# Kernel optimization log

Hardware: AMD Instinct MI355X
Metric: run time of the kernel (lower is better)

Reference implementation:

```python
import jax, jax.numpy as jnp
import numpy as np

E = 6          # num_experts
TOP_K = 2
FUT = 60       # future_len
DIM = 128

def _gelu(x):
    return jax.nn.gelu(x, approximate=False)  # torch nn.GELU default is exact erf


def setup_inputs() -> dict:
    key = jax.random.key(0)
    ks = jax.random.split(key, 20)
    B, M, D = 8192, 6, DIM
    s = 0.02
    inp = {
        "mode_features": jax.random.normal(ks[0], (B, M, D), jnp.float32),
        # router MLP: D->256->128->E  (dropout is identity in eval mode)
        "rW1": jax.random.normal(ks[1], (D, 256)) * s, "rb1": jnp.zeros((256,)),
        "rW2": jax.random.normal(ks[2], (256, 128)) * s, "rb2": jnp.zeros((128,)),
        "rW3": jax.random.normal(ks[3], (128, E)) * s, "rb3": jnp.zeros((E,)),
        # stacked expert trajectory heads: D->256->256->2*FUT
        "tW1": jax.random.normal(ks[4], (E, D, 256)) * s, "tb1": jnp.zeros((E, 256)),
        "tW2": jax.random.normal(ks[5], (E, 256, 256)) * s, "tb2": jnp.zeros((E, 256)),
        "tW3": jax.random.normal(ks[6], (E, 256, 2 * FUT)) * s, "tb3": jnp.zeros((E, 2 * FUT)),
        # stacked expert score heads: D->128->64->1
        "sW1": jax.random.normal(ks[7], (E, D, 128)) * s, "sb1": jnp.zeros((E, 128)),
        "sW2": jax.random.normal(ks[8], (E, 128, 64)) * s, "sb2": jnp.zeros((E, 64)),
        "sW3": jax.random.normal(ks[9], (E, 64, 1)) * s, "sb3": jnp.zeros((E, 1)),
    }
    return {k: v.astype(jnp.float32) for k, v in inp.items()}


def reference(mode_features, rW1, rb1, rW2, rb2, rW3, rb3,
              tW1, tb1, tW2, tb2, tW3, tb3,
              sW1, sb1, sW2, sb2, sW3, sb3):
    B, M, D = mode_features.shape
    x = mode_features.reshape(B * M, D)  # [N, D]

    # ---- router (dropout = identity at inference) ----
    h = _gelu(x @ rW1 + rb1)
    h = _gelu(h @ rW2 + rb2)
    logits = h @ rW3 + rb3                      # [N, E]
    router_probs = jax.nn.softmax(logits, axis=-1)

    top_v, top_i = jax.lax.top_k(logits, TOP_K)  # [N, K]
    top_w = jax.nn.softmax(top_v, axis=-1)       # renormalized top-k weights

    # ---- all experts, dense over E (then gather top-k) ----
    th = _gelu(jnp.einsum('nd,edh->neh', x, tW1) + tb1)   # [N, E, 256]
    th = _gelu(jnp.einsum('neh,ehg->neg', th, tW2) + tb2) # [N, E, 256]
    traj_all = jnp.einsum('neh,eho->neo', th, tW3) + tb3  # [N, E, 2*FUT]

    sh = _gelu(jnp.einsum('nd,edh->neh', x, sW1) + sb1)   # [N, E, 128]
    sh = _gelu(jnp.einsum('neh,ehg->neg', sh, sW2) + sb2) # [N, E, 64]
    score_all = (jnp.einsum('neh,eho->neo', sh, sW3) + sb3)[..., 0]  # [N, E]

    traj_sel = jnp.take_along_axis(traj_all, top_i[:, :, None], axis=1)  # [N, K, 2*FUT]
    score_sel = jnp.take_along_axis(score_all, top_i, axis=1)            # [N, K]

    trajectories = (top_w[:, :, None] * traj_sel).sum(axis=1).reshape(B, M, FUT, 2)
    scores = (top_w * score_sel).sum(axis=1).reshape(B, M)

    # ---- load-balance aux loss ----
    avg_probs = router_probs.mean(axis=0)  # [E]
    entropy = -(avg_probs * jnp.log(avg_probs + 1e-8)).sum()
    lb_loss = -entropy * 0.01
    l2_loss = jnp.mean((avg_probs - 1.0 / E) ** 2)
    aux_loss = lb_loss + 0.01 * l2_loss

    return trajectories, scores, aux_loss, router_probs.reshape(B, M, E)
```

## Files before the change

kernel.cpp:

```cpp
#include <hip/hip_runtime.h>

#define N_TOK 49152
#define PER_E 155648
#define NSTAGE 19
#define RSTAGES 24

#define TRAJ_OFF 0
#define SCORE_OFF 5898240
#define AUX_OFF  5947392
#define PROB_OFF 5947393

typedef __attribute__((ext_vector_type(8))) short short8v;
typedef __attribute__((ext_vector_type(4))) float f32x4;
typedef __attribute__((ext_vector_type(4))) unsigned short u16x4;

typedef __attribute__((address_space(3))) unsigned char lds_byte;
typedef __attribute__((address_space(1))) const unsigned char gl_byte;

__device__ __forceinline__ unsigned short f2bf(float f) {
  unsigned int u = __float_as_uint(f);
  u = (u + 0x7FFFu + ((u >> 16) & 1u)) >> 16;
  return (unsigned short)u;
}
__device__ __forceinline__ float bf2f(unsigned short h) {
  return __uint_as_float(((unsigned int)h) << 16);
}
__device__ __forceinline__ float geluf(float v) {
  float x = v * 0.70710678118654752f;
  float ax = fabsf(x);
  float t = __builtin_amdgcn_rcpf(fmaf(0.3275911f, ax, 1.0f));
  float p = t * fmaf(t, fmaf(t, fmaf(t, fmaf(t, 1.061405429f, -1.453152027f),
                                     1.421413741f), -0.284496736f), 0.254829592f);
  float er = 1.0f - p * __expf(-ax * ax);
  er = copysignf(er, x);
  return 0.5f * v * (1.0f + er);
}

__global__ __launch_bounds__(256) void prep_weights(
    const float* __restrict__ tW1, const float* __restrict__ tW2, const float* __restrict__ tW3,
    const float* __restrict__ sW1, const float* __restrict__ sW2,
    unsigned short* __restrict__ blob)
{
  int id = blockIdx.x * 256 + threadIdx.x;
  if (id >= 6 * PER_E) return;
  int e = id / PER_E;
  int r = id - e * PER_E;
  int p = r >> 13;
  int q = r & 8191;
  int f = q >> 9;
  int l = (q >> 3) & 63;
  int j = q & 7;
  int hi = l >> 4, rl = l & 15;
  const float* src; int N, tile, ks; bool perm;
  if (p < 2)       { src = sW1 + e * 16384; N = 128; tile = 4 * p + (f >> 2);        ks = f & 3; perm = false; }
  else if (p == 2) { src = sW2 + e * 8192;  N = 64;  tile = f >> 2;                  ks = f & 3; perm = true;  }
  else if (p < 7)  { src = tW1 + e * 32768; N = 256; tile = 4 * (p - 3) + (f >> 2);  ks = f & 3; perm = false; }
  else if (p < 11) { src = tW2 + e * 65536; N = 256; tile = 2 * (p - 7) + (f >> 3);  ks = f & 7; perm = true;  }
  else if (p < 13) { src = tW3 + e * 30720; N = 120; tile = f >> 1;  ks = 2 * (p - 11) + (f & 1); perm = true; }
  else if (p < 17) { src = tW2 + e * 65536; N = 256; tile = 8 + 2 * (p - 13) + (f >> 3); ks = f & 7; perm = true; }
  else             { src = tW3 + e * 30720; N = 120; tile = f >> 1;  ks = 4 + 2 * (p - 17) + (f & 1); perm = true; }
  int k = ks * 32 + (perm ? (16 * (j >> 2) + 4 * hi + (j & 3)) : (8 * hi + j));
  int unit = tile * 16 + rl;
  blob[id] = f2bf(unit < N ? src[k * N + unit] : 0.0f);
}

__global__ __launch_bounds__(256) void prep_router(
    const float* __restrict__ rW1, const float* __restrict__ rW2,
    unsigned short* __restrict__ rblob)
{
  int id = blockIdx.x * 256 + threadIdx.x;
  if (id >= RSTAGES * 8192) return;
  int p = id >> 13;
  int q = id & 8191;
  int f = q >> 9;
  int l = (q >> 3) & 63;
  int j = q & 7;
  int hi = l >> 4, rl = l & 15;
  const float* src; int N, tile, ks, part; bool perm;
  if (p < 12) { int c = p / 3; part = p % 3; src = rW1; N = 256; tile = 4 * c + (f >> 2); ks = f & 3; perm = false; }
  else        { int c = (p - 12) / 3; part = (p - 12) % 3; src = rW2; N = 128; tile = 2 * c + (f >> 3); ks = f & 7; perm = true; }
  int k = ks * 32 + (perm ? (16 * (j >> 2) + 4 * hi + (j & 3)) : (8 * hi + j));
  int unit = tile * 16 + rl;
  float v = (unit < N) ? src[k * N + unit] : 0.0f;
  unsigned short b0 = f2bf(v);
  float r1 = v - bf2f(b0);
  unsigned short b1 = f2bf(r1);
  float r2 = r1 - bf2f(b1);
  unsigned short b2 = f2bf(r2);
  rblob[id] = (part == 0) ? b0 : ((part == 1) ? b1 : b2);
}

__device__ __forceinline__ f32x4 MM16(short8v a, short8v b, f32x4 c) {
  return __builtin_amdgcn_mfma_f32_16x16x32_bf16(a, b, c, 0, 0, 0);
}
__device__ __forceinline__ void cvt16(f32x4 aE, f32x4 aO, const float* bp, int hi, short8v& fr) {
  #pragma unroll
  for (int j = 0; j < 8; ++j) {
    float v = (j < 4) ? aE[j & 3] : aO[j & 3];
    int unit = 16 * (j >> 2) + 4 * hi + (j & 3);
    fr[j] = (short)f2bf(geluf(v + bp[unit]));
  }
}
__device__ __forceinline__ void cvt16s(f32x4 aE, f32x4 aO, const float* bp, int hi,
                                       short8v& f0, short8v& f1) {
  #pragma unroll
  for (int j = 0; j < 8; ++j) {
    float v = (j < 4) ? aE[j & 3] : aO[j & 3];
    int unit = 16 * (j >> 2) + 4 * hi + (j & 3);
    float g = geluf(v + bp[unit]);
    unsigned short b0 = f2bf(g);
    f0[j] = (short)b0;
    f1[j] = (short)f2bf(g - bf2f(b0));
  }
}

#define FRAG(s, f) (*(const short8v*)(&wlds[((s) % 3) * 8192 + (f) * 512 + lane * 8]))

#define RSTAGE(s) do { \
    const unsigned short* gsrc_ = rblob + (s) * 8192 + w * 1024 + lane * 8; \
    unsigned short* ldst_ = &wlds[((s) % 3) * 8192 + w * 1024]; \
    _Pragma("unroll") \
    for (int i_ = 0; i_ < 2; ++i_) \
      __builtin_amdgcn_global_load_lds((gl_byte*)(gsrc_ + i_ * 512), (lds_byte*)(ldst_ + i_ * 512), 16, 0, 0); \
  } while (0)

#define RPIPE(s, nw) do { \
    asm volatile("s_waitcnt vmcnt(" #nw ")" ::: "memory"); \
    __builtin_amdgcn_sched_barrier(0); \
    __builtin_amdgcn_s_barrier(); \
    __builtin_amdgcn_sched_barrier(0); \
    if ((s) + 2 < RSTAGES) RSTAGE((s) + 2); \
  } while (0)

__global__ __launch_bounds__(512, 4) void router_mfma(
    const float* __restrict__ x, const unsigned short* __restrict__ rblob,
    const float* __restrict__ rb1, const float* __restrict__ rb2,
    const float* __restrict__ rW3, const float* __restrict__ rb3,
    float* __restrict__ probs_out,
    int* __restrict__ pairTok, float* __restrict__ pairW, int* __restrict__ pairIdx,
    int* __restrict__ cnt, float* __restrict__ probsum)
{
  __shared__ __align__(16) unsigned short wlds[3 * 8192];
  __shared__ float bLds[1160];
  __shared__ float probsLds[768];
  __shared__ float psum[8];
  __shared__ int lcnt[8], gbase[8];

  int tid = threadIdx.x;
  int lane = tid & 63;
  int w = tid >> 6;
  int col = lane & 15;
  int hi = lane >> 4;
  int tok0 = blockIdx.x * 128;
  int myTok = tok0 + w * 16 + col;

  if (tid < 256) bLds[tid] = rb1[tid];
  else if (tid < 384) bLds[tid] = rb2[tid - 256];
  for (int i = tid; i < 768; i += 512) bLds[384 + i] = rW3[i];
  if (tid < 6) bLds[1152 + tid] = rb3[tid];
  if (tid < 8) { psum[tid] = 0.f; lcnt[tid] = 0; }

  short8v xf0[4], xf1[4], xf2[4];
  {
    const float* px = x + (size_t)myTok * 128 + hi * 8;
    #pragma unroll
    for (int ks = 0; ks < 4; ++ks) {
      f32x4 lo = *(const f32x4*)(px + ks * 32);
      f32x4 hv = *(const f32x4*)(px + ks * 32 + 4);
      #pragma unroll
      for (int j = 0; j < 8; ++j) {
        float v = (j < 4) ? lo[j & 3] : hv[j & 3];
        unsigned short b0 = f2bf(v);
        float r1 = v - bf2f(b0);
        unsigned short b1 = f2bf(r1);
        float r2 = r1 - bf2f(b1);
        xf0[ks][j] = (short)b0;
        xf1[ks][j] = (short)b1;
        xf2[ks][j] = (short)f2bf(r2);
      }
    }
  }
  __syncthreads();

  RSTAGE(0);
  RSTAGE(1);

  short8v h0B[8], h1B[8];
  #pragma unroll
  for (int c = 0; c < 4; ++c) {
    f32x4 acc[4] = {};
    RPIPE(3 * c, 2);
    #pragma unroll
    for (int ks = 0; ks < 4; ++ks)
      #pragma unroll
      for (int u = 0; u < 4; ++u) {
        short8v wf = FRAG(3 * c, u * 4 + ks);
        acc[u] = MM16(wf, xf0[ks], acc[u]);
        acc[u] = MM16(wf, xf1[ks], acc[u]);
        acc[u] = MM16(wf, xf2[ks], acc[u]);
      }
    RPIPE(3 * c + 1, 2);
    #pragma unroll
    for (int ks = 0; ks < 4; ++ks)
      #pragma unroll
      for (int u = 0; u < 4; ++u) {
        short8v wf = FRAG(3 * c + 1, u * 4 + ks);
        acc[u] = MM16(wf, xf0[ks], acc[u]);
        acc[u] = MM16(wf, xf1[ks], acc[u]);
      }
    RPIPE(3 * c + 2, 2);
    #pragma unroll
    for (int ks = 0; ks < 4; ++ks)
      #pragma unroll
      for (int u = 0; u < 4; ++u) {
        short8v wf = FRAG(3 * c + 2, u * 4 + ks);
        acc[u] = MM16(wf, xf0[ks], acc[u]);
      }
    cvt16s(acc[0], acc[1], bLds + 32 * (2 * c),     hi, h0B[2 * c],     h1B[2 * c]);
    cvt16s(acc[2], acc[3], bLds + 32 * (2 * c + 1), hi, h0B[2 * c + 1], h1B[2 * c + 1]);
  }

  f32x4 acc2[8] = {};
  #pragma unroll
  for (int d = 0; d < 4; ++d) {
    RPIPE(12 + 3 * d, 2);
    #pragma unroll
    for (int ks = 0; ks < 8; ++ks)
      #pragma unroll
      for (int u = 0; u < 2; ++u) {
        short8v wf = FRAG(12 + 3 * d, u * 8 + ks);
        int t = 2 * d + u;
        acc2[t] = MM16(wf, h0B[ks], acc2[t]);
        acc2[t] = MM16(wf, h1B[ks], acc2[t]);
      }
    RPIPE(12 + 3 * d + 1, 2);
    #pragma unroll
    for (int ks = 0; ks < 8; ++ks)
      #pragma unroll
      for (int u = 0; u < 2; ++u) {
        short8v wf = FRAG(12 + 3 * d + 1, u * 8 + ks);
        int t = 2 * d + u;
        acc2[t] = MM16(wf, h0B[ks], acc2[t]);
        acc2[t] = MM16(wf, h1B[ks], acc2[t]);
      }
    if (d < 3) { RPIPE(12 + 3 * d + 2, 2); }
    else       { RPIPE(23, 0); }
    #pragma unroll
    for (int ks = 0; ks < 8; ++ks)
      #pragma unroll
      for (int u = 0; u < 2; ++u) {
        short8v wf = FRAG(12 + 3 * d + 2, u * 8 + ks);
        int t = 2 * d + u;
        acc2[t] = MM16(wf, h0B[ks], acc2[t]);
      }
  }

  float pl[6] = {0.f, 0.f, 0.f, 0.f, 0.f, 0.f};
  #pragma unroll
  for (int t = 0; t < 8; ++t)
    #pragma unroll
    for (int r = 0; r < 4; ++r) {
      int unit = t * 16 + 4 * hi + r;
      float h2 = geluf(acc2[t][r] + bLds[256 + unit]);
      #pragma unroll
      for (int e = 0; e < 6; ++e)
        pl[e] = fmaf(h2, bLds[384 + unit * 6 + e], pl[e]);
    }
  #pragma unroll
  for (int e = 0; e < 6; ++e) {
    pl[e] += __shfl_xor(pl[e], 16);
    pl[e] += __shfl_xor(pl[e], 32);
  }

  int i1 = 0, i2 = 0, lp1 = 0, lp2 = 0;
  float ww1 = 0.f, ww2 = 0.f;
  if (hi == 0) {
    float l0[6];
    #pragma unroll
    for (int e = 0; e < 6; ++e) l0[e] = pl[e] + bLds[1152 + e];
    float m = l0[0];
    #pragma unroll
    for (int e = 1; e < 6; ++e) m = fmaxf(m, l0[e]);
    float pe[6]; float ssum = 0.f;
    #pragma unroll
    for (int e = 0; e < 6; ++e) { pe[e] = expf(l0[e] - m); ssum += pe[e]; }
    float inv = 1.f / ssum;
    int lrow = w * 16 + col;
    #pragma unroll
    for (int e = 0; e < 6; ++e) {
      float prb = pe[e] * inv;
      probsLds[lrow * 6 + e] = prb;
      atomicAdd(&psum[e], prb);
    }
    float v1 = l0[0]; i1 = 0; float v2 = -1e30f; i2 = -1;
    #pragma unroll
    for (int e = 1; e < 6; ++e) {
      float v = l0[e];
      if (v > v1) { v2 = v1; i2 = i1; v1 = v; i1 = e; }
      else if (v > v2) { v2 = v; i2 = e; }
    }
    float e2 = expf(v2 - v1);
    float den = 1.f / (1.f + e2);
    ww1 = den; ww2 = e2 * den;
    lp1 = atomicAdd(&lcnt[i1], 1);
    lp2 = atomicAdd(&lcnt[i2], 1);
  }
  __syncthreads();
  if (tid < 6) gbase[tid] = atomicAdd(&cnt[tid], lcnt[tid]);
  __syncthreads();
  if (hi == 0) {
    int g1 = gbase[i1] + lp1, g2 = gbase[i2] + lp2;
    pairTok[i1 * N_TOK + g1] = myTok; pairW[i1 * N_TOK + g1] = ww1;
    pairTok[i2 * N_TOK + g2] = myTok; pairW[i2 * N_TOK + g2] = ww2;
    pairIdx[2 * myTok]     = i1 * N_TOK + g1;
    pairIdx[2 * myTok + 1] = i2 * N_TOK + g2;
  }
  if (tid < 6) atomicAdd(&probsum[tid], psum[tid]);
  for (int i = tid; i < 768; i += 512)
    probs_out[(size_t)tok0 * 6 + i] = probsLds[i];
}

__global__ void aux_kernel(const float* __restrict__ probsum, const int* __restrict__ cnt,
                           int* __restrict__ csum, float* __restrict__ auxout)
{
  if (threadIdx.x == 0 && blockIdx.x == 0) {
    int s = 0;
    for (int e = 0; e < 6; ++e) { csum[e] = s; s += cnt[e]; }
    float ent = 0.f, l2 = 0.f;
    for (int e = 0; e < 6; ++e) {
      float avg = probsum[e] / (float)N_TOK;
      ent -= avg * logf(avg + 1e-8f);
      float d = avg - (1.0f / 6.0f);
      l2 += d * d;
    }
    l2 *= (1.0f / 6.0f);
    auxout[0] = -ent * 0.01f + 0.01f * l2;
  }
}

#define STAGE(s) do { \
    const unsigned short* gsrc_ = eblob + (s) * 8192 + w * 1024 + lane * 8; \
    unsigned short* ldst_ = &wlds[((s) % 3) * 8192 + w * 1024]; \
    _Pragma("unroll") \
    for (int i_ = 0; i_ < 2; ++i_) \
      __builtin_amdgcn_global_load_lds((gl_byte*)(gsrc_ + i_ * 512), (lds_byte*)(ldst_ + i_ * 512), 16, 0, 0); \
  } while (0)

#define PIPE(s, nw) do { \
    asm volatile("s_waitcnt vmcnt(" #nw ")" ::: "memory"); \
    __builtin_amdgcn_sched_barrier(0); \
    __builtin_amdgcn_s_barrier(); \
    __builtin_amdgcn_sched_barrier(0); \
    if ((s) + 2 < NSTAGE) STAGE((s) + 2); \
  } while (0)

template<int OUTMODE>
__global__ __launch_bounds__(512, 4) void expert_kernel(
    const float* __restrict__ x,
    const unsigned short* __restrict__ blob,
    const float* __restrict__ tb1, const float* __restrict__ tb2, const float* __restrict__ tb3,
    const float* __restrict__ sb1, const float* __restrict__ sb2,
    const float* __restrict__ sW3, const float* __restrict__ sb3,
    const int* __restrict__ pairTok, const float* __restrict__ pairW,
    const int* __restrict__ cnt, const int* __restrict__ csum,
    float* __restrict__ traj_out, float* __restrict__ score_out,
    unsigned short* __restrict__ trajP, float* __restrict__ scoreP)
{
  int e = blockIdx.y;
  int base = blockIdx.x * 128;
  int count = cnt[e];
  if (base >= count) return;

  __shared__ __align__(16) unsigned short wlds[3 * 8192];
  __shared__ float bLds[896];
  __shared__ int   toksLds[128];
  __shared__ float gwsLds[128];

  int tid = threadIdx.x;
  int lane = tid & 63;
  int w = tid >> 6;
  int col = lane & 15;
  int hi = lane >> 4;
  const unsigned short* eblob = blob + (size_t)e * PER_E;
  int slotbase = csum[e] + base;

  if (tid < 128) {
    int idx = e * N_TOK + base + ((base + tid < count) ? tid : 0);
    toksLds[tid] = pairTok[idx];
    gwsLds[tid] = (base + tid < count) ? pairW[idx] : 0.f;
  }
  if (tid < 128) bLds[tid] = sb1[e * 128 + tid];
  if (tid < 64)  bLds[128 + tid] = sb2[e * 64 + tid];
  if (tid < 64)  bLds[192 + tid] = sW3[e * 64 + tid];
  if (tid < 256) { bLds[256 + tid] = tb1[e * 256 + tid]; bLds[512 + tid] = tb2[e * 256 + tid]; }
  if (tid < 120) bLds[768 + tid] = tb3[e * 120 + tid];
  __syncthreads();

  int row = w * 16 + col;
  int tok = toksLds[row];
  bool valid = (base + row < count);
  float gw = gwsLds[row];

  short8v xf[4];
  {
    const float* px = x + (size_t)tok * 128 + hi * 8;
    #pragma unroll
    for (int ks = 0; ks < 4; ++ks) {
      f32x4 lo = *(const f32x4*)(px + ks * 32);
      f32x4 hv = *(const f32x4*)(px + ks * 32 + 4);
      short8v t;
      #pragma unroll
      for (int j = 0; j < 4; ++j) { t[j] = (short)f2bf(lo[j]); t[4 + j] = (short)f2bf(hv[j]); }
      xf[ks] = t;
    }
  }

  STAGE(0);
  STAGE(1);

  short8v sB[4];
  {
    f32x4 a[4] = {};
    PIPE(0, 2);
    #pragma unroll
    for (int f = 0; f < 16; ++f)
      a[f >> 2] = MM16(FRAG(0, f), xf[f & 3], a[f >> 2]);
    cvt16(a[0], a[1], bLds + 0,  hi, sB[0]);  cvt16(a[2], a[3], bLds + 32, hi, sB[1]);
    f32x4 b[4] = {};
    PIPE(1, 2);
    #pragma unroll
    for (int f = 0; f < 16; ++f)
      b[f >> 2] = MM16(FRAG(1, f), xf[f & 3], b[f >> 2]);
    cvt16(b[0], b[1], bLds + 64, hi, sB[2]);  cvt16(b[2], b[3], bLds + 96, hi, sB[3]);
  }

  float p0 = 0.f;
  {
    f32x4 q[4] = {};
    PIPE(2, 2);
    #pragma unroll
    for (int f = 0; f < 16; ++f)
      q[f >> 2] = MM16(FRAG(2, f), sB[f & 3], q[f >> 2]);
    #pragma unroll
    for (int t = 0; t < 4; ++t)
      #pragma unroll
      for (int r = 0; r < 4; ++r) {
        int unit = t * 16 + 4 * hi + r;
        p0 += geluf(q[t][r] + bLds[128 + unit]) * bLds[192 + unit];
      }
    p0 += __shfl_xor(p0, 16); p0 += __shfl_xor(p0, 32);
  }

  short8v h1B[8];
  #define T1S(t, S) { \
    f32x4 a[4] = {}; \
    PIPE(S, 2); \
    _Pragma("unroll") \
    for (int f = 0; f < 16; ++f) \
      a[f >> 2] = MM16(FRAG(S, f), xf[f & 3], a[f >> 2]); \
    cvt16(a[0], a[1], bLds + 256 + (t) * 64,      hi, h1B[2 * (t)]); \
    cvt16(a[2], a[3], bLds + 256 + (t) * 64 + 32, hi, h1B[2 * (t) + 1]); \
  }
  T1S(0, 3) T1S(1, 4) T1S(2, 5) T1S(3, 6)

  short8v h2B[4];
  #define T2S(s, S, BOFF) { \
    f32x4 u[2] = {}; \
    PIPE(S, 2); \
    _Pragma("unroll") \
    for (int f = 0; f < 16; ++f) \
      u[f >> 3] = MM16(FRAG(S, f), h1B[f & 7], u[f >> 3]); \
    cvt16(u[0], u[1], bLds + 512 + (BOFF) + 32 * (s), hi, h2B[s]); \
  }

  f32x4 wacc[8] = {};
  #define T3S(s, S, NW) { \
    PIPE(S, NW); \
    _Pragma("unroll") \
    for (int f = 0; f < 16; ++f) \
      wacc[f >> 1] = MM16(FRAG(S, f), h2B[2 * (s) + (f & 1)], wacc[f >> 1]); \
  }

  T2S(0, 7, 0) T2S(1, 8, 0) T2S(2, 9, 0) T2S(3, 10, 0)
  T3S(0, 11, 2) T3S(1, 12, 2)
  T2S(0, 13, 128) T2S(1, 14, 128) T2S(2, 15, 128) T2S(3, 16, 128)
  T3S(0, 17, 2) T3S(1, 18, 0)

  if (hi == 0 && valid) {
    float v = gw * (p0 + sb3[e]);
    if (OUTMODE == 0) scoreP[slotbase + row] = v; else atomicAdd(&score_out[tok], v);
  }
  if (valid) {
    if (OUTMODE == 0) {
      unsigned short* dst = trajP + (size_t)(slotbase + row) * 120;
      #pragma unroll
      for (int t = 0; t < 8; ++t)
        #pragma unroll
        for (int r = 0; r < 4; r += 2) {
          int unit = t * 16 + 4 * hi + r;
          if (unit + 1 < 120) {
            float a0 = gw * (wacc[t][r] + bLds[768 + unit]);
            float a1 = gw * (wacc[t][r + 1] + bLds[768 + unit + 1]);
            *(unsigned int*)(dst + unit) = (unsigned)f2bf(a0) | ((unsigned)f2bf(a1) << 16);
          }
        }
    } else {
      float* dst = traj_out + (size_t)tok * 120;
      #pragma unroll
      for (int t = 0; t < 8; ++t)
        #pragma unroll
        for (int r = 0; r < 4; ++r) {
          int unit = t * 16 + 4 * hi + r;
          if (unit < 120) atomicAdd(&dst[unit], gw * (wacc[t][r] + bLds[768 + unit]));
        }
    }
  }
}

__global__ __launch_bounds__(256) void combine_kernel(
    const int* __restrict__ pairIdx, const int* __restrict__ csum,
    const unsigned short* __restrict__ trajP, const float* __restrict__ scoreP,
    float* __restrict__ traj_out, float* __restrict__ score_out)
{
  int t = blockIdx.x * 256 + threadIdx.x;
  if (t >= N_TOK) return;
  int p0 = pairIdx[2 * t], p1 = pairIdx[2 * t + 1];
  int e0 = p0 / N_TOK, e1 = p1 / N_TOK;
  size_t s0 = (size_t)csum[e0] + (p0 - e0 * N_TOK);
  size_t s1 = (size_t)csum[e1] + (p1 - e1 * N_TOK);
  const unsigned short* r0 = trajP + s0 * 120;
  const unsigned short* r1 = trajP + s1 * 120;
  float* o = traj_out + (size_t)t * 120;
  #pragma unroll 6
  for (int i = 0; i < 30; ++i) {
    u16x4 a = *(const u16x4*)(r0 + i * 4);
    u16x4 b = *(const u16x4*)(r1 + i * 4);
    f32x4 v;
    #pragma unroll
    for (int jj = 0; jj < 4; ++jj) v[jj] = bf2f(a[jj]) + bf2f(b[jj]);
    *(f32x4*)(o + i * 4) = v;
  }
  score_out[t] = scoreP[s0] + scoreP[s1];
}

extern "C" void kernel_launch(void* const* d_in, const int* in_sizes, int n_in,
                              void* d_out, int out_size, void* d_ws, size_t ws_size,
                              hipStream_t stream) {
  (void)in_sizes; (void)n_in; (void)out_size;
  const float* x   = (const float*)d_in[0];
  const float* rW1 = (const float*)d_in[1];
  const float* rb1 = (const float*)d_in[2];
  const float* rW2 = (const float*)d_in[3];
  const float* rb2 = (const float*)d_in[4];
  const float* rW3 = (const float*)d_in[5];
  const float* rb3 = (const float*)d_in[6];
  const float* tW1 = (const float*)d_in[7];
  const float* tb1 = (const float*)d_in[8];
  const float* tW2 = (const float*)d_in[9];
  const float* tb2 = (const float*)d_in[10];
  const float* tW3 = (const float*)d_in[11];
  const float* tb3 = (const float*)d_in[12];
  const float* sW1 = (const float*)d_in[13];
  const float* sb1 = (const float*)d_in[14];
  const float* sW2 = (const float*)d_in[15];
  const float* sb2 = (const float*)d_in[16];
  const float* sW3 = (const float*)d_in[17];
  const float* sb3 = (const float*)d_in[18];
  float* out = (float*)d_out;

  char* wsb = (char*)d_ws;
  int*   cnt     = (int*)(wsb + 0);
  float* probsum = (float*)(wsb + 32);
  int*   csum    = (int*)(wsb + 64);
  int*   pairTok = (int*)(wsb + 96);
  float* pairW   = (float*)(wsb + 96 + (size_t)6 * N_TOK * 4);
  int*   pairIdx = (int*)(wsb + 96 + (size_t)12 * N_TOK * 4);
  float* scoreP  = (float*)(wsb + 96 + (size_t)14 * N_TOK * 4);
  unsigned short* blob  = (unsigned short*)(wsb + 96 + (size_t)16 * N_TOK * 4);
  unsigned short* rblob = (unsigned short*)(wsb + 96 + (size_t)16 * N_TOK * 4 + (size_t)6 * PER_E * 2);
  unsigned short* trajP = (unsigned short*)(wsb + 96 + (size_t)16 * N_TOK * 4 + (size_t)6 * PER_E * 2
                                            + (size_t)RSTAGES * 8192 * 2);
  size_t need = 96 + (size_t)16 * N_TOK * 4 + (size_t)6 * PER_E * 2 + (size_t)RSTAGES * 8192 * 2
              + (size_t)2 * N_TOK * 120 * 2;
  bool scratch = ws_size >= need;

  hipMemsetAsync(wsb, 0, 96, stream);
  if (!scratch) hipMemsetAsync(d_out, 0, (size_t)(N_TOK * 121) * 4, stream);

  prep_weights<<<(6 * PER_E) / 256, 256, 0, stream>>>(tW1, tW2, tW3, sW1, sW2, blob);
  prep_router<<<(RSTAGES * 8192) / 256, 256, 0, stream>>>(rW1, rW2, rblob);
  router_mfma<<<N_TOK / 128, 512, 0, stream>>>(x, rblob, rb1, rb2, rW3, rb3,
                                               out + PROB_OFF, pairTok, pairW, pairIdx, cnt, probsum);
  aux_kernel<<<1, 64, 0, stream>>>(probsum, cnt, csum, out + AUX_OFF);
  if (scratch) {
    expert_kernel<0><<<dim3(N_TOK / 128, 6), 512, 0, stream>>>(
        x, blob, tb1, tb2, tb3, sb1, sb2, sW3, sb3, pairTok, pairW, cnt, csum,
        out + TRAJ_OFF, out + SCORE_OFF, trajP, scoreP);
    combine_kernel<<<N_TOK / 256, 256, 0, stream>>>(pairIdx, csum, trajP, scoreP,
                                                    out + TRAJ_OFF, out + SCORE_OFF);
  } else {
    expert_kernel<1><<<dim3(N_TOK / 128, 6), 512, 0, stream>>>(
        x, blob, tb1, tb2, tb3, sb1, sb2, sW3, sb3, pairTok, pairW, cnt, csum,
        out + TRAJ_OFF, out + SCORE_OFF, trajP, scoreP);
  }
}
```

Before: 174.1 us.

## Compact expert tile list, use cheaper GELU, and packed bf16 conversion

The expert launch changes from a dense 384x6 grid, where most blocks exited early, to a compact 1D list of (expert, tile) entries built in the aux kernel. This removes the launch and scheduling of empty blocks. GELU inside the expert MLPs now uses a lower-order erf approximation, and the float-to-bf16 conversions use the hardware packed instruction v_cvt_pk_bf16_f32 in place of manual rounding. The cheaper erf and packed conversion lower VALU work but slightly reduce accuracy.

```diff
diff --git a/kernel.cpp b/kernel.cpp
--- a/kernel.cpp
+++ b/kernel.cpp
@@ -4,6 +4,7 @@
 #define PER_E 155648
 #define NSTAGE 19
 #define RSTAGES 24
+#define MAXTILES 774
 
 #define TRAJ_OFF 0
 #define SCORE_OFF 5898240
@@ -24,6 +25,11 @@
 }
 __device__ __forceinline__ float bf2f(unsigned short h) {
   return __uint_as_float(((unsigned int)h) << 16);
+}
+__device__ __forceinline__ unsigned int pkbf(float a, float b) {
+  unsigned int r;
+  asm("v_cvt_pk_bf16_f32 %0, %1, %2" : "=v"(r) : "v"(a), "v"(b));
+  return r;
 }
 __device__ __forceinline__ float geluf(float v) {
   float x = v * 0.70710678118654752f;
@@ -32,6 +38,15 @@
   float p = t * fmaf(t, fmaf(t, fmaf(t, fmaf(t, 1.061405429f, -1.453152027f),
                                      1.421413741f), -0.284496736f), 0.254829592f);
   float er = 1.0f - p * __expf(-ax * ax);
+  er = copysignf(er, x);
+  return 0.5f * v * (1.0f + er);
+}
+__device__ __forceinline__ float geluf_fast(float v) {
+  float x = v * 0.70710678f;
+  float ax = fabsf(x);
+  float t = __builtin_amdgcn_rcpf(fmaf(0.47047f, ax, 1.0f));
+  float poly = t * fmaf(t, fmaf(t, 0.7478556f, -0.0958798f), 0.3480242f);
+  float er = fmaf(-poly, __expf(-ax * ax), 1.0f);
   er = copysignf(er, x);
   return 0.5f * v * (1.0f + er);
 }
@@ -94,12 +109,16 @@
   return __builtin_amdgcn_mfma_f32_16x16x32_bf16(a, b, c, 0, 0, 0);
 }
 __device__ __forceinline__ void cvt16(f32x4 aE, f32x4 aO, const float* bp, int hi, short8v& fr) {
+  float g[8];
   #pragma unroll
   for (int j = 0; j < 8; ++j) {
     float v = (j < 4) ? aE[j & 3] : aO[j & 3];
     int unit = 16 * (j >> 2) + 4 * hi + (j & 3);
-    fr[j] = (short)f2bf(geluf(v + bp[unit]));
-  }
+    g[j] = geluf_fast(v + bp[unit]);
+  }
+  unsigned int* pr = (unsigned int*)&fr;
+  pr[0] = pkbf(g[0], g[1]); pr[1] = pkbf(g[2], g[3]);
+  pr[2] = pkbf(g[4], g[5]); pr[3] = pkbf(g[6], g[7]);
 }
 __device__ __forceinline__ void cvt16s(f32x4 aE, f32x4 aO, const float* bp, int hi,
                                        short8v& f0, short8v& f1) {
@@ -321,11 +340,17 @@
 }
 
 __global__ void aux_kernel(const float* __restrict__ probsum, const int* __restrict__ cnt,
-                           int* __restrict__ csum, float* __restrict__ auxout)
+                           int* __restrict__ csum, int* __restrict__ ntiles, int* __restrict__ tiles,
+                           float* __restrict__ auxout)
 {
   if (threadIdx.x == 0 && blockIdx.x == 0) {
     int s = 0;
     for (int e = 0; e < 6; ++e) { csum[e] = s; s += cnt[e]; }
+    int nt = 0;
+    for (int e = 0; e < 6; ++e)
+      for (int b = 0; b < cnt[e]; b += 128)
+        tiles[nt++] = (e << 16) | (b >> 7);
+    ntiles[0] = nt;
     float ent = 0.f, l2 = 0.f;
     for (int e = 0; e < 6; ++e) {
       float avg = probsum[e] / (float)N_TOK;
@@ -363,13 +388,15 @@
     const float* __restrict__ sW3, const float* __restrict__ sb3,
     const int* __restrict__ pairTok, const float* __restrict__ pairW,
     const int* __restrict__ cnt, const int* __restrict__ csum,
+    const int* __restrict__ ntiles, const int* __restrict__ tiles,
     float* __restrict__ traj_out, float* __restrict__ score_out,
     unsigned short* __restrict__ trajP, float* __restrict__ scoreP)
 {
-  int e = blockIdx.y;
-  int base = blockIdx.x * 128;
+  if (blockIdx.x >= (unsigned)ntiles[0]) return;
+  int ent = tiles[blockIdx.x];
+  int e = ent >> 16;
+  int base = (ent & 0xffff) << 7;
   int count = cnt[e];
-  if (base >= count) return;
 
   __shared__ __align__(16) unsigned short wlds[3 * 8192];
   __shared__ float bLds[896];
@@ -408,10 +435,9 @@
     for (int ks = 0; ks < 4; ++ks) {
       f32x4 lo = *(const f32x4*)(px + ks * 32);
       f32x4 hv = *(const f32x4*)(px + ks * 32 + 4);
-      short8v t;
-      #pragma unroll
-      for (int j = 0; j < 4; ++j) { t[j] = (short)f2bf(lo[j]); t[4 + j] = (short)f2bf(hv[j]); }
-      xf[ks] = t;
+      unsigned int* pt = (unsigned int*)&xf[ks];
+      pt[0] = pkbf(lo[0], lo[1]); pt[1] = pkbf(lo[2], lo[3]);
+      pt[2] = pkbf(hv[0], hv[1]); pt[3] = pkbf(hv[2], hv[3]);
     }
   }
 
@@ -446,7 +472,7 @@
       #pragma unroll
       for (int r = 0; r < 4; ++r) {
         int unit = t * 16 + 4 * hi + r;
-        p0 += geluf(q[t][r] + bLds[128 + unit]) * bLds[192 + unit];
+        p0 += geluf_fast(q[t][r] + bLds[128 + unit]) * bLds[192 + unit];
       }
     p0 += __shfl_xor(p0, 16); p0 += __shfl_xor(p0, 32);
   }
@@ -501,7 +527,7 @@
           if (unit + 1 < 120) {
             float a0 = gw * (wacc[t][r] + bLds[768 + unit]);
             float a1 = gw * (wacc[t][r + 1] + bLds[768 + unit + 1]);
-            *(unsigned int*)(dst + unit) = (unsigned)f2bf(a0) | ((unsigned)f2bf(a1) << 16);
+            *(unsigned int*)(dst + unit) = pkbf(a0, a1);
           }
         }
     } else {
@@ -572,35 +598,38 @@
   int*   cnt     = (int*)(wsb + 0);
   float* probsum = (float*)(wsb + 32);
   int*   csum    = (int*)(wsb + 64);
-  int*   pairTok = (int*)(wsb + 96);
-  float* pairW   = (float*)(wsb + 96 + (size_t)6 * N_TOK * 4);
-  int*   pairIdx = (int*)(wsb + 96 + (size_t)12 * N_TOK * 4);
-  float* scoreP  = (float*)(wsb + 96 + (size_t)14 * N_TOK * 4);
-  unsigned short* blob  = (unsigned short*)(wsb + 96 + (size_t)16 * N_TOK * 4);
-  unsigned short* rblob = (unsigned short*)(wsb + 96 + (size_t)16 * N_TOK * 4 + (size_t)6 * PER_E * 2);
-  unsigned short* trajP = (unsigned short*)(wsb + 96 + (size_t)16 * N_TOK * 4 + (size_t)6 * PER_E * 2
+  int*   ntiles  = (int*)(wsb + 96);
+  int*   tiles   = (int*)(wsb + 112);
+  const size_t B = 112 + 4 * ((MAXTILES + 7) & ~7);
+  int*   pairTok = (int*)(wsb + B);
+  float* pairW   = (float*)(wsb + B + (size_t)6 * N_TOK * 4);
+  int*   pairIdx = (int*)(wsb + B + (size_t)12 * N_TOK * 4);
+  float* scoreP  = (float*)(wsb + B + (size_t)14 * N_TOK * 4);
+  unsigned short* blob  = (unsigned short*)(wsb + B + (size_t)16 * N_TOK * 4);
+  unsigned short* rblob = (unsigned short*)(wsb + B + (size_t)16 * N_TOK * 4 + (size_t)6 * PER_E * 2);
+  unsigned short* trajP = (unsigned short*)(wsb + B + (size_t)16 * N_TOK * 4 + (size_t)6 * PER_E * 2
                                             + (size_t)RSTAGES * 8192 * 2);
-  size_t need = 96 + (size_t)16 * N_TOK * 4 + (size_t)6 * PER_E * 2 + (size_t)RSTAGES * 8192 * 2
+  size_t need = B + (size_t)16 * N_TOK * 4 + (size_t)6 * PER_E * 2 + (size_t)RSTAGES * 8192 * 2
               + (size_t)2 * N_TOK * 120 * 2;
   bool scratch = ws_size >= need;
 
-  hipMemsetAsync(wsb, 0, 96, stream);
+  hipMemsetAsync(wsb, 0, 112, stream);
   if (!scratch) hipMemsetAsync(d_out, 0, (size_t)(N_TOK * 121) * 4, stream);
 
   prep_weights<<<(6 * PER_E) / 256, 256, 0, stream>>>(tW1, tW2, tW3, sW1, sW2, blob);
   prep_router<<<(RSTAGES * 8192) / 256, 256, 0, stream>>>(rW1, rW2, rblob);
   router_mfma<<<N_TOK / 128, 512, 0, stream>>>(x, rblob, rb1, rb2, rW3, rb3,
                                                out + PROB_OFF, pairTok, pairW, pairIdx, cnt, probsum);
-  aux_kernel<<<1, 64, 0, stream>>>(probsum, cnt, csum, out + AUX_OFF);
+  aux_kernel<<<1, 64, 0, stream>>>(probsum, cnt, csum, ntiles, tiles, out + AUX_OFF);
   if (scratch) {
-    expert_kernel<0><<<dim3(N_TOK / 128, 6), 512, 0, stream>>>(
-        x, blob, tb1, tb2, tb3, sb1, sb2, sW3, sb3, pairTok, pairW, cnt, csum,
+    expert_kernel<0><<<MAXTILES, 512, 0, stream>>>(
+        x, blob, tb1, tb2, tb3, sb1, sb2, sW3, sb3, pairTok, pairW, cnt, csum, ntiles, tiles,
         out + TRAJ_OFF, out + SCORE_OFF, trajP, scoreP);
     combine_kernel<<<N_TOK / 256, 256, 0, stream>>>(pairIdx, csum, trajP, scoreP,
                                                     out + TRAJ_OFF, out + SCORE_OFF);
   } else {
-    expert_kernel<1><<<dim3(N_TOK / 128, 6), 512, 0, stream>>>(
-        x, blob, tb1, tb2, tb3, sb1, sb2, sW3, sb3, pairTok, pairW, cnt, csum,
+    expert_kernel<1><<<MAXTILES, 512, 0, stream>>>(
+        x, blob, tb1, tb2, tb3, sb1, sb2, sW3, sb3, pairTok, pairW, cnt, csum, ntiles, tiles,
         out + TRAJ_OFF, out + SCORE_OFF, trajP, scoreP);
   }
 }
```

New measurement: 178.8 us. 1.03x slower.
